# Optimization experiments

Measured on AMD Instinct MI355X. Metric: run time of the kernel, lower is better.

## Reference

```python
import jax, jax.numpy as jnp
import numpy as np

B, T, D = 8, 2048, 1024

def _xavier(key, shape):
    fan_in, fan_out = shape[1], shape[0]
    limit = float(np.sqrt(6.0 / (fan_in + fan_out)))
    return jax.random.uniform(key, shape, jnp.float32, -limit, limit)

def setup_inputs() -> dict:
    key = jax.random.key(0)
    ks = jax.random.split(key, 6)
    x = jax.random.normal(ks[0], (B, T, D), jnp.float32)
    return {
        "x": x,
        "h0": jnp.zeros((B, D), jnp.float32),
        "W_in": _xavier(ks[1], (D, D)),      # in_proj.weight [d_inner, dim]
        "W_alpha": _xavier(ks[2], (D, D)),
        "d_alpha": jnp.full((D,), 0.1, jnp.float32),
        "b_alpha": jnp.full((D,), 2.0, jnp.float32),
        "W_x": _xavier(ks[3], (D, D)),
        "b_v": jnp.zeros((D,), jnp.float32),
        "W_out": _xavier(ks[4], (D, D)),     # out_proj.weight [dim, d_inner]
    }

def _silu(u):
    return u * jax.nn.sigmoid(u)

def reference(x, h0, W_in, W_alpha, d_alpha, b_alpha, W_x, b_v, W_out):
    # in_proj + SiLU: [B,T,D]
    x_proj = _silu(jnp.einsum('btd,ed->bte', x, W_in))
    # to [T,B,D] for the scan
    x_rnn = jnp.transpose(x_proj, (1, 0, 2))
    # precompute per-step gate/value GEMM contributions (as in torch ref)
    alpha_x = jnp.einsum('tbd,ed->tbe', x_rnn, W_alpha)          # [T,B,D]
    v_all = jnp.tanh(jnp.einsum('tbd,ed->tbe', x_rnn, W_x) + b_v)  # [T,B,D]

    def step(h_prev, inputs):
        ax_t, v_t = inputs
        alpha = jax.nn.sigmoid(ax_t + d_alpha * h_prev + b_alpha)
        h_new = alpha * h_prev + (1.0 - alpha) * v_t
        out_t = h_new * _silu(h_new)
        return h_new, out_t

    h_final, cell_out = jax.lax.scan(step, h0, (alpha_x, v_all))  # cell_out: [T,B,D]
    cell_out = jnp.transpose(cell_out, (1, 0, 2))                 # [B,T,D]
    output = jnp.einsum('btd,ed->bte', cell_out, W_out)
    return output, h_final
```

## Files before the change

### kernel.cpp

```cpp
#include <hip/hip_runtime.h>
#include <hip/hip_bf16.h>

typedef __attribute__((ext_vector_type(8))) short short8;
typedef __attribute__((ext_vector_type(4))) short short4v;
typedef __attribute__((ext_vector_type(4))) float f32x4;

#define Dk 1024
#define TT 2048
#define BB 8
#define MROWS (BB * TT)
#define LOG2E 1.44269504088896f

#if defined(__has_builtin)
#if __has_builtin(__builtin_amdgcn_rcpf)
#define FAST_RCP(x) __builtin_amdgcn_rcpf(x)
#endif
#if __has_builtin(__builtin_amdgcn_exp2f)
#define FAST_EXP2(x) __builtin_amdgcn_exp2f(x)
#endif
#endif
#ifndef FAST_RCP
#define FAST_RCP(x) (1.f / (x))
#endif
#ifndef FAST_EXP2
#define FAST_EXP2(x) exp2f(x)
#endif

#define BAR()   __builtin_amdgcn_s_barrier()
#define LGKM0() do { asm volatile("s_waitcnt lgkmcnt(0)" ::: "memory"); \
                     __builtin_amdgcn_sched_barrier(0); } while (0)

__device__ __forceinline__ void gload_lds16(const void* g, void* l) {
    __builtin_amdgcn_global_load_lds(
        (const __attribute__((address_space(1))) void*)g,
        (__attribute__((address_space(3))) void*)l, 16, 0, 0);
}

__device__ __forceinline__ float sigmoidf_fast(float x) {
    return FAST_RCP(1.f + FAST_EXP2(-x * LOG2E));
}

__device__ __forceinline__ unsigned short bf16_bits(float x) {
    union { __hip_bfloat16 h; unsigned short u; } c;
    c.h = __float2bfloat16(x);
    return c.u;
}

__global__ __launch_bounds__(256)
void cvt_all(const float* __restrict__ x,
             const float* __restrict__ w0, const float* __restrict__ w1,
             const float* __restrict__ w2, const float* __restrict__ w3,
             __hip_bfloat16* __restrict__ xo,
             __hip_bfloat16* __restrict__ o0, __hip_bfloat16* __restrict__ o1,
             __hip_bfloat16* __restrict__ o2, __hip_bfloat16* __restrict__ o3)
{
    const int bid = blockIdx.x;
    const float* in;
    __hip_bfloat16* out;
    int base;
    if (bid < 16384) {
        in = x; out = xo; base = bid * 1024;
    } else {
        const int wbid  = bid - 16384;
        const int which = wbid >> 10;
        in  = which == 0 ? w0 : which == 1 ? w1 : which == 2 ? w2 : w3;
        out = which == 0 ? o0 : which == 1 ? o1 : which == 2 ? o2 : o3;
        base = (wbid & 1023) * 1024;
    }
    const int i = base + threadIdx.x * 4;
    const float4 v = *(const float4*)(in + i);
    __hip_bfloat16 tmp[4];
    tmp[0] = __float2bfloat16(v.x);
    tmp[1] = __float2bfloat16(v.y);
    tmp[2] = __float2bfloat16(v.z);
    tmp[3] = __float2bfloat16(v.w);
    *(short4v*)(out + i) = *(const short4v*)tmp;
}

template<int EPI>
__global__ __launch_bounds__(512)
void gemm256(const __hip_bfloat16* __restrict__ A,
             const __hip_bfloat16* __restrict__ Bw,
             const float* __restrict__ bias,
             const float* __restrict__ dal,
             void* __restrict__ CoutV)
{
    __shared__ __align__(16) char lds[2 * 65536];

    const int tid  = threadIdx.x;
    const int bid  = blockIdx.x;
    const int nbid = (bid & 7) * 32 + (bid >> 3);
    const int tn   = nbid & 3;
    const int tm   = nbid >> 2;
    const int lane = tid & 63;
    const int w    = tid >> 6;
    const int wm   = w >> 2;
    const int wn   = w & 3;
    const int l15  = lane & 15;
    const int lq   = lane >> 4;

    const __hip_bfloat16* Ap = A  + (size_t)(tm * 256) * Dk;
    const __hip_bfloat16* Bp = Bw + (size_t)(tn * 256) * Dk;

    const int rA = wm * 16384 + l15 * 128;
    const int rB = 32768 + wn * 8192 + l15 * 128;
    int c8k[2];
    c8k[0] = ((lq    ) ^ (l15 & 7)) * 16;
    c8k[1] = ((lq + 4) ^ (l15 & 7)) * 16;

    const int srow = tid >> 3;
    const int scol = ((tid & 7) ^ (srow & 7)) * 8;

    auto stageHalf = [&](const __hip_bfloat16* src0, int reg, int h, int kt, int bb) {
#pragma unroll
        for (int j = 0; j < 2; ++j) {
            const int row  = h * 128 + j * 64 + srow;
            const int slot = h * 1024 + j * 512 + tid;
            gload_lds16(src0 + (size_t)row * Dk + kt * 64 + scol,
                        (char*)lds + bb + reg * 32768 + slot * 16);
        }
    };

    f32x4 acc[8][4];
#pragma unroll
    for (int m = 0; m < 8; ++m)
#pragma unroll
        for (int n = 0; n < 4; ++n)
            acc[m][n] = (f32x4){0.f, 0.f, 0.f, 0.f};

    stageHalf(Ap, 0, 0, 0, 0);      stageHalf(Ap, 0, 1, 0, 0);
    stageHalf(Bp, 1, 0, 0, 0);      stageHalf(Bp, 1, 1, 0, 0);
    stageHalf(Bp, 1, 0, 1, 65536);  stageHalf(Bp, 1, 1, 1, 65536);
    asm volatile("s_waitcnt vmcnt(4)" ::: "memory");
    BAR();

    short8 a[4][2], bfr[4][2];

    for (int t = 0; t < 16; ++t) {
        const int bb = (t & 1) * 65536;
        const int nb = bb ^ 65536;
        const char* cb = (const char*)lds + bb;

#pragma unroll
        for (int m = 0; m < 4; ++m)
#pragma unroll
            for (int kk = 0; kk < 2; ++kk)
                a[m][kk] = *(const short8*)(cb + rA + m * 2048 + c8k[kk]);
#pragma unroll
        for (int n = 0; n < 2; ++n)
#pragma unroll
            for (int kk = 0; kk < 2; ++kk)
                bfr[n][kk] = *(const short8*)(cb + rB + n * 2048 + c8k[kk]);
        if (t + 1 < 16) stageHalf(Ap, 0, 0, t + 1, nb);
        BAR(); LGKM0();
        __builtin_amdgcn_s_setprio(1);
#pragma unroll
        for (int m = 0; m < 4; ++m)
#pragma unroll
            for (int n = 0; n < 2; ++n)
#pragma unroll
                for (int kk = 0; kk < 2; ++kk)
                    acc[m][n] = __builtin_amdgcn_mfma_f32_16x16x32_bf16(
                        a[m][kk], bfr[n][kk], acc[m][n], 0, 0, 0);
        __builtin_amdgcn_s_setprio(0);
        BAR();

#pragma unroll
        for (int n = 2; n < 4; ++n)
#pragma unroll
            for (int kk = 0; kk < 2; ++kk)
                bfr[n][kk] = *(const short8*)(cb + rB + n * 2048 + c8k[kk]);
        if (t + 1 < 16) stageHalf(Ap, 0, 1, t + 1, nb);
        BAR(); LGKM0();
        __builtin_amdgcn_s_setprio(1);
#pragma unroll
        for (int m = 0; m < 4; ++m)
#pragma unroll
            for (int n = 2; n < 4; ++n)
#pragma unroll
                for (int kk = 0; kk < 2; ++kk)
                    acc[m][n] = __builtin_amdgcn_mfma_f32_16x16x32_bf16(
                        a[m][kk], bfr[n][kk], acc[m][n], 0, 0, 0);
        __builtin_amdgcn_s_setprio(0);
        BAR();

#pragma unroll
        for (int m = 0; m < 4; ++m)
#pragma unroll
            for (int kk = 0; kk < 2; ++kk)
                a[m][kk] = *(const short8*)(cb + rA + (m + 4) * 2048 + c8k[kk]);
        if (t + 2 < 16) stageHalf(Bp, 1, 0, t + 2, bb);
        BAR(); LGKM0();
        __builtin_amdgcn_s_setprio(1);
#pragma unroll
        for (int m = 0; m < 4; ++m)
#pragma unroll
            for (int n = 0; n < 2; ++n)
#pragma unroll
                for (int kk = 0; kk < 2; ++kk)
                    acc[m + 4][n] = __builtin_amdgcn_mfma_f32_16x16x32_bf16(
                        a[m][kk], bfr[n][kk], acc[m + 4][n], 0, 0, 0);
        __builtin_amdgcn_s_setprio(0);
        BAR();

        if (t + 2 < 16) stageHalf(Bp, 1, 1, t + 2, bb);
        BAR();
        __builtin_amdgcn_s_setprio(1);
#pragma unroll
        for (int m = 0; m < 4; ++m)
#pragma unroll
            for (int n = 2; n < 4; ++n)
#pragma unroll
                for (int kk = 0; kk < 2; ++kk)
                    acc[m + 4][n] = __builtin_amdgcn_mfma_f32_16x16x32_bf16(
                        a[m][kk], bfr[n][kk], acc[m + 4][n], 0, 0, 0);
        __builtin_amdgcn_s_setprio(0);
        if (t < 14) {
            asm volatile("s_waitcnt vmcnt(4)" ::: "memory");
        } else if (t == 14) {
            asm volatile("s_waitcnt vmcnt(0)" ::: "memory");
        }
        BAR();
    }

#pragma unroll
    for (int m = 0; m < 8; ++m) {
#pragma unroll
        for (int n = 0; n < 4; ++n) {
            const int col = tn * 256 + wn * 64 + n * 16 + l15;
            float bv_ = 0.f;
            if (EPI == 6 || EPI == 7) bv_ = bias[col];
#pragma unroll
            for (int j = 0; j < 4; ++j) {
                const int rowg = tm * 256 + wm * 128 + m * 16 + lq * 4 + j;
                const size_t idx = (size_t)rowg * Dk + col;
                const float xv = acc[m][n][j];
                if constexpr (EPI == 0) {
                    ((__hip_bfloat16*)CoutV)[idx] =
                        __float2bfloat16(xv * sigmoidf_fast(xv));
                } else if constexpr (EPI == 1) {
                    ((float*)CoutV)[idx] = xv;
                } else if constexpr (EPI == 6) {
                    const float e = FAST_EXP2(-(xv + bv_) * LOG2E);
                    ((unsigned short*)CoutV)[idx * 2] = bf16_bits(e);
                } else {
                    const float y = xv + bv_;
                    const float e = FAST_EXP2(fabsf(y) * (2.f * LOG2E));
                    float tv = 1.f - 2.f * FAST_RCP(e + 1.f);
                    tv = copysignf(tv, y);
                    float nl2 = -dal[col] * LOG2E;
                    if (fabsf(nl2) < 1e-18f) nl2 = -1e-18f;
                    ((unsigned short*)CoutV)[idx * 2 + 1] = bf16_bits(tv * nl2);
                }
            }
        }
    }
}

#define HPAD 68
__global__ __launch_bounds__(192)
void scan_kernel(const unsigned int* __restrict__ EV,
                 const float* __restrict__ h0,
                 const float* __restrict__ dal,
                 __hip_bfloat16* __restrict__ cell, float* __restrict__ hfin)
{
    constexpr int CH  = 64;
    constexpr int NCH = TT / CH;
    __shared__ __align__(16) unsigned int lEV[2][CH * 64];
    __shared__ __align__(16) float        lHT[2][64 * HPAD];

    const int tid  = threadIdx.x;
    const int wave = tid >> 6;
    const int lane = tid & 63;
    const int bx   = blockIdx.x;
    const int b    = bx >> 4;
    const int d0   = (bx & 15) * 64;
    const int d    = d0 + lane;
    const int g    = b * Dk + d;

    float nl2 = -dal[d] * LOG2E;
    if (fabsf(nl2) < 1e-18f) nl2 = -1e-18f;
    const float inv_nl2 = 1.f / nl2;

    const size_t sbase = (size_t)b * TT * Dk + d0;

    if (wave == 0) {
        float ht = h0[g] * nl2;

        const int sl = lane >> 4;
        const int co = (lane & 15) * 4;
        auto issue = [&](int ck, int buf) {
#pragma unroll
            for (int grp = 0; grp < 16; ++grp) {
                const size_t off = sbase + (size_t)(ck * CH + grp * 4 + sl) * Dk + co;
                gload_lds16(EV + off, (void*)&lEV[buf][grp * 256]);
            }
        };

        issue(0, 0);
        for (int k = 0; k < NCH; ++k) {
            const int buf = k & 1;
            asm volatile("s_waitcnt vmcnt(0)" ::: "memory");
            if (k + 1 < NCH) issue(k + 1, buf ^ 1);
            __builtin_amdgcn_sched_barrier(0);

#pragma unroll
            for (int g8 = 0; g8 < 8; ++g8) {
                unsigned int wv[8];
#pragma unroll
                for (int j = 0; j < 8; ++j)
                    wv[j] = lEV[buf][(g8 * 8 + j) * 64 + lane];
                float hts[8];
#pragma unroll
                for (int j = 0; j < 8; ++j) {
                    const float E  = __uint_as_float(wv[j] << 16);
                    const float Vt = __uint_as_float(wv[j] & 0xffff0000u);
                    const float u  = FAST_EXP2(ht);
                    const float al = FAST_RCP(fmaf(E, u, 1.f));
                    ht = fmaf(al, ht - Vt, Vt);
                    hts[j] = ht;
                }
                *(f32x4*)&lHT[buf][lane * HPAD + g8 * 8] =
                    (f32x4){hts[0], hts[1], hts[2], hts[3]};
                *(f32x4*)&lHT[buf][lane * HPAD + g8 * 8 + 4] =
                    (f32x4){hts[4], hts[5], hts[6], hts[7]};
            }
            asm volatile("s_waitcnt lgkmcnt(0)" ::: "memory");
            __builtin_amdgcn_s_barrier();
        }
        hfin[g] = ht * inv_nl2;
    } else {
        const float c1   = -inv_nl2 * LOG2E;
        const float inv2 = inv_nl2 * inv_nl2;
        const int   s0   = (wave - 1) * 32;
        for (int k = 0; k < NCH; ++k) {
            __builtin_amdgcn_s_barrier();
            const int buf = k & 1;
            const size_t cbase = sbase + (size_t)(k * CH) * Dk + lane;
#pragma unroll
            for (int g8 = 0; g8 < 4; ++g8) {
                const int s = s0 + g8 * 8;
                const f32x4 h0v = *(const f32x4*)&lHT[buf][lane * HPAD + s];
                const f32x4 h1v = *(const f32x4*)&lHT[buf][lane * HPAD + s + 4];
                float htv[8] = {h0v[0], h0v[1], h0v[2], h0v[3],
                                h1v[0], h1v[1], h1v[2], h1v[3]};
#pragma unroll
                for (int j = 0; j < 8; ++j) {
                    const float ht = htv[j];
                    const float sg = FAST_RCP(1.f + FAST_EXP2(ht * c1));
                    cell[cbase + (size_t)(s + j) * Dk] =
                        __float2bfloat16(ht * ht * inv2 * sg);
                }
            }
        }
    }
}

extern "C" void kernel_launch(void* const* d_in, const int* in_sizes, int n_in,
                              void* d_out, int out_size, void* d_ws, size_t ws_size,
                              hipStream_t stream)
{
    const float* x     = (const float*)d_in[0];
    const float* h0    = (const float*)d_in[1];
    const float* W_in  = (const float*)d_in[2];
    const float* W_al  = (const float*)d_in[3];
    const float* d_al  = (const float*)d_in[4];
    const float* b_al  = (const float*)d_in[5];
    const float* W_x   = (const float*)d_in[6];
    const float* b_v   = (const float*)d_in[7];
    const float* W_out = (const float*)d_in[8];

    float* out  = (float*)d_out;
    float* hfin = out + (size_t)MROWS * Dk;

    char* ws = (char*)d_ws;
    const size_t bfBuf = (size_t)MROWS * Dk * sizeof(__hip_bfloat16);
    const size_t wBuf  = (size_t)Dk * Dk * sizeof(__hip_bfloat16);

    __hip_bfloat16* xb    = (__hip_bfloat16*)(ws);
    __hip_bfloat16* Winb  = (__hip_bfloat16*)(ws + bfBuf);
    __hip_bfloat16* Walb  = (__hip_bfloat16*)(ws + bfBuf + wBuf);
    __hip_bfloat16* Wxb   = (__hip_bfloat16*)(ws + bfBuf + 2 * wBuf);
    __hip_bfloat16* Woutb = (__hip_bfloat16*)(ws + bfBuf + 3 * wBuf);
    char* rest = ws + bfBuf + 4 * wBuf;
    __hip_bfloat16* xproj = (__hip_bfloat16*)rest;
    unsigned int*   EVb   = (unsigned int*)(rest + bfBuf);

    __hip_bfloat16* cellb = xproj;

    dim3 blk(256);
    cvt_all<<<dim3(16384 + 4096), blk, 0, stream>>>(
        x, W_in, W_al, W_x, W_out, xb, Winb, Walb, Wxb, Woutb);

    dim3 gblk(512), ggrid(256);
    gemm256<0><<<ggrid, gblk, 0, stream>>>(xb,    Winb,  nullptr, nullptr, xproj);
    gemm256<6><<<ggrid, gblk, 0, stream>>>(xproj, Walb,  b_al,    nullptr, EVb);
    gemm256<7><<<ggrid, gblk, 0, stream>>>(xproj, Wxb,   b_v,     d_al,    EVb);
    scan_kernel<<<dim3(128), dim3(192), 0, stream>>>(EVb, h0, d_al, cellb, hfin);
    gemm256<1><<<ggrid, gblk, 0, stream>>>(cellb, Woutb, nullptr, nullptr, out);
}
```

Before: 243.1 us.

## Split E/V buffers and give each scan wave two independent channel chains

E and Vt are no longer interleaved into one 32-bit word. The two gate GEMMs now write separate contiguous bf16 arrays. The scan kernel handles 128 channels per block with 64 blocks instead of 128, so the scan wave runs two independent recurrence chains per lane to hide exp/rcp latency. Each of the two consumer waves now handles 64 channels across all 64 steps. The cost is half as many blocks on the GPU, which means lower parallelism across CUs, plus more LDS use per block.

```diff
diff --git a/kernel.cpp b/kernel.cpp
--- a/kernel.cpp
+++ b/kernel.cpp
@@ -242,7 +242,7 @@
                     ((float*)CoutV)[idx] = xv;
                 } else if constexpr (EPI == 6) {
                     const float e = FAST_EXP2(-(xv + bv_) * LOG2E);
-                    ((unsigned short*)CoutV)[idx * 2] = bf16_bits(e);
+                    ((__hip_bfloat16*)CoutV)[idx] = __float2bfloat16(e);
                 } else {
                     const float y = xv + bv_;
                     const float e = FAST_EXP2(fabsf(y) * (2.f * LOG2E));
@@ -250,7 +250,7 @@
                     tv = copysignf(tv, y);
                     float nl2 = -dal[col] * LOG2E;
                     if (fabsf(nl2) < 1e-18f) nl2 = -1e-18f;
-                    ((unsigned short*)CoutV)[idx * 2 + 1] = bf16_bits(tv * nl2);
+                    ((__hip_bfloat16*)CoutV)[idx] = __float2bfloat16(tv * nl2);
                 }
             }
         }
@@ -259,41 +259,45 @@
 
 #define HPAD 68
 __global__ __launch_bounds__(192)
-void scan_kernel(const unsigned int* __restrict__ EV,
+void scan_kernel(const __hip_bfloat16* __restrict__ Eb,
+                 const __hip_bfloat16* __restrict__ Vtb,
                  const float* __restrict__ h0,
                  const float* __restrict__ dal,
                  __hip_bfloat16* __restrict__ cell, float* __restrict__ hfin)
 {
     constexpr int CH  = 64;
     constexpr int NCH = TT / CH;
-    __shared__ __align__(16) unsigned int lEV[2][CH * 64];
-    __shared__ __align__(16) float        lHT[2][64 * HPAD];
+    __shared__ __align__(16) unsigned short lE [2][CH * 128];
+    __shared__ __align__(16) unsigned short lVt[2][CH * 128];
+    __shared__ __align__(16) float lHT[2][128 * HPAD];
 
     const int tid  = threadIdx.x;
     const int wave = tid >> 6;
     const int lane = tid & 63;
     const int bx   = blockIdx.x;
-    const int b    = bx >> 4;
-    const int d0   = (bx & 15) * 64;
-    const int d    = d0 + lane;
-    const int g    = b * Dk + d;
-
-    float nl2 = -dal[d] * LOG2E;
-    if (fabsf(nl2) < 1e-18f) nl2 = -1e-18f;
-    const float inv_nl2 = 1.f / nl2;
+    const int b    = bx >> 3;
+    const int d0   = (bx & 7) * 128;
 
     const size_t sbase = (size_t)b * TT * Dk + d0;
 
     if (wave == 0) {
-        float ht = h0[g] * nl2;
+        const int da = d0 + lane, db = da + 64;
+        const int ga = b * Dk + da, gb = ga + 64;
+        float nl2a = -dal[da] * LOG2E;
+        if (fabsf(nl2a) < 1e-18f) nl2a = -1e-18f;
+        float nl2b = -dal[db] * LOG2E;
+        if (fabsf(nl2b) < 1e-18f) nl2b = -1e-18f;
+        float ht0 = h0[ga] * nl2a;
+        float ht1 = h0[gb] * nl2b;
 
         const int sl = lane >> 4;
-        const int co = (lane & 15) * 4;
+        const int co = (lane & 15) * 8;
         auto issue = [&](int ck, int buf) {
 #pragma unroll
             for (int grp = 0; grp < 16; ++grp) {
                 const size_t off = sbase + (size_t)(ck * CH + grp * 4 + sl) * Dk + co;
-                gload_lds16(EV + off, (void*)&lEV[buf][grp * 256]);
+                gload_lds16(Eb  + off, (void*)&lE [buf][grp * 512]);
+                gload_lds16(Vtb + off, (void*)&lVt[buf][grp * 512]);
             }
         };
 
@@ -306,49 +310,65 @@
 
 #pragma unroll
             for (int g8 = 0; g8 < 8; ++g8) {
-                unsigned int wv[8];
-#pragma unroll
-                for (int j = 0; j < 8; ++j)
-                    wv[j] = lEV[buf][(g8 * 8 + j) * 64 + lane];
-                float hts[8];
+                float h0s[8], h1s[8];
 #pragma unroll
                 for (int j = 0; j < 8; ++j) {
-                    const float E  = __uint_as_float(wv[j] << 16);
-                    const float Vt = __uint_as_float(wv[j] & 0xffff0000u);
-                    const float u  = FAST_EXP2(ht);
-                    const float al = FAST_RCP(fmaf(E, u, 1.f));
-                    ht = fmaf(al, ht - Vt, Vt);
-                    hts[j] = ht;
+                    const int s = g8 * 8 + j;
+                    const float E0 = __uint_as_float(
+                        (unsigned)lE [buf][s * 128 + lane] << 16);
+                    const float V0 = __uint_as_float(
+                        (unsigned)lVt[buf][s * 128 + lane] << 16);
+                    const float E1 = __uint_as_float(
+                        (unsigned)lE [buf][s * 128 + 64 + lane] << 16);
+                    const float V1 = __uint_as_float(
+                        (unsigned)lVt[buf][s * 128 + 64 + lane] << 16);
+                    const float u0 = FAST_EXP2(ht0);
+                    const float u1 = FAST_EXP2(ht1);
+                    const float a0 = FAST_RCP(fmaf(E0, u0, 1.f));
+                    const float a1 = FAST_RCP(fmaf(E1, u1, 1.f));
+                    ht0 = fmaf(a0, ht0 - V0, V0);
+                    ht1 = fmaf(a1, ht1 - V1, V1);
+                    h0s[j] = ht0;
+                    h1s[j] = ht1;
                 }
                 *(f32x4*)&lHT[buf][lane * HPAD + g8 * 8] =
-                    (f32x4){hts[0], hts[1], hts[2], hts[3]};
+                    (f32x4){h0s[0], h0s[1], h0s[2], h0s[3]};
                 *(f32x4*)&lHT[buf][lane * HPAD + g8 * 8 + 4] =
-                    (f32x4){hts[4], hts[5], hts[6], hts[7]};
+                    (f32x4){h0s[4], h0s[5], h0s[6], h0s[7]};
+                *(f32x4*)&lHT[buf][(64 + lane) * HPAD + g8 * 8] =
+                    (f32x4){h1s[0], h1s[1], h1s[2], h1s[3]};
+                *(f32x4*)&lHT[buf][(64 + lane) * HPAD + g8 * 8 + 4] =
+                    (f32x4){h1s[4], h1s[5], h1s[6], h1s[7]};
             }
             asm volatile("s_waitcnt lgkmcnt(0)" ::: "memory");
             __builtin_amdgcn_s_barrier();
         }
-        hfin[g] = ht * inv_nl2;
+        hfin[ga] = ht0 / nl2a;
+        hfin[gb] = ht1 / nl2b;
     } else {
-        const float c1   = -inv_nl2 * LOG2E;
-        const float inv2 = inv_nl2 * inv_nl2;
-        const int   s0   = (wave - 1) * 32;
+        const int dl = (wave - 1) * 64 + lane;
+        const int dc = d0 + dl;
+        float nl2 = -dal[dc] * LOG2E;
+        if (fabsf(nl2) < 1e-18f) nl2 = -1e-18f;
+        const float inv  = 1.f / nl2;
+        const float c1   = -inv * LOG2E;
+        const float inv2 = inv * inv;
+
         for (int k = 0; k < NCH; ++k) {
             __builtin_amdgcn_s_barrier();
             const int buf = k & 1;
-            const size_t cbase = sbase + (size_t)(k * CH) * Dk + lane;
-#pragma unroll
-            for (int g8 = 0; g8 < 4; ++g8) {
-                const int s = s0 + g8 * 8;
-                const f32x4 h0v = *(const f32x4*)&lHT[buf][lane * HPAD + s];
-                const f32x4 h1v = *(const f32x4*)&lHT[buf][lane * HPAD + s + 4];
-                float htv[8] = {h0v[0], h0v[1], h0v[2], h0v[3],
-                                h1v[0], h1v[1], h1v[2], h1v[3]};
+            const size_t cb2 = sbase + (size_t)(k * CH) * Dk + dl;
+#pragma unroll
+            for (int g8 = 0; g8 < 8; ++g8) {
+                const f32x4 v0 = *(const f32x4*)&lHT[buf][dl * HPAD + g8 * 8];
+                const f32x4 v1 = *(const f32x4*)&lHT[buf][dl * HPAD + g8 * 8 + 4];
+                float hv[8] = {v0[0], v0[1], v0[2], v0[3],
+                               v1[0], v1[1], v1[2], v1[3]};
 #pragma unroll
                 for (int j = 0; j < 8; ++j) {
-                    const float ht = htv[j];
+                    const float ht = hv[j];
                     const float sg = FAST_RCP(1.f + FAST_EXP2(ht * c1));
-                    cell[cbase + (size_t)(s + j) * Dk] =
+                    cell[cb2 + (size_t)(g8 * 8 + j) * Dk] =
                         __float2bfloat16(ht * ht * inv2 * sg);
                 }
             }
@@ -384,7 +404,8 @@
     __hip_bfloat16* Woutb = (__hip_bfloat16*)(ws + bfBuf + 3 * wBuf);
     char* rest = ws + bfBuf + 4 * wBuf;
     __hip_bfloat16* xproj = (__hip_bfloat16*)rest;
-    unsigned int*   EVb   = (unsigned int*)(rest + bfBuf);
+    __hip_bfloat16* Ebuf  = (__hip_bfloat16*)(rest + bfBuf);
+    __hip_bfloat16* Vtbuf = (__hip_bfloat16*)(rest + 2 * bfBuf);
 
     __hip_bfloat16* cellb = xproj;
 
@@ -394,8 +415,9 @@
 
     dim3 gblk(512), ggrid(256);
     gemm256<0><<<ggrid, gblk, 0, stream>>>(xb,    Winb,  nullptr, nullptr, xproj);
-    gemm256<6><<<ggrid, gblk, 0, stream>>>(xproj, Walb,  b_al,    nullptr, EVb);
-    gemm256<7><<<ggrid, gblk, 0, stream>>>(xproj, Wxb,   b_v,     d_al,    EVb);
-    scan_kernel<<<dim3(128), dim3(192), 0, stream>>>(EVb, h0, d_al, cellb, hfin);
+    gemm256<6><<<ggrid, gblk, 0, stream>>>(xproj, Walb,  b_al,    nullptr, Ebuf);
+    gemm256<7><<<ggrid, gblk, 0, stream>>>(xproj, Wxb,   b_v,     d_al,    Vtbuf);
+    scan_kernel<<<dim3(64), dim3(192), 0, stream>>>(Ebuf, Vtbuf, h0, d_al,
+                                                    cellb, hfin);
     gemm256<1><<<ggrid, gblk, 0, stream>>>(cellb, Woutb, nullptr, nullptr, out);
 }
```

After: 293.3 us. 1.21x slower.
